# Kernel optimization log

Measured on AMD Instinct MI355X. Metric: run time of the kernel, lower is better.

## Reference

```python
import jax, jax.numpy as jnp
import numpy as np

S, N, D, H = 1024, 8, 1024, 16
DK = D // H
SCALE = np.sqrt(DK).astype(np.float32)


def setup_inputs() -> dict:
    key = jax.random.key(0)
    ks = jax.random.split(key, 16)
    f32 = jnp.float32
    Qpoi = jax.random.normal(ks[0], (S, N, D), f32)
    Qsvi = jax.random.normal(ks[1], (S, N, D), f32)
    K = jax.random.normal(ks[2], (S, N, D), f32)
    V = jax.random.normal(ks[3], (S, N, D), f32)
    # padding mask: True = masked key; random valid lengths in [S//2, S]
    lengths = jax.random.randint(ks[4], (N,), S // 2, S + 1)
    key_padding_mask = jnp.arange(S)[None, :] >= lengths[:, None]  # [N, S] bool
    w = 0.02
    wq_poi_w = jax.random.normal(ks[5], (D, D), f32) * w
    wq_poi_b = jnp.zeros((D,), f32)
    wq_svi_w = jax.random.normal(ks[6], (D, D), f32) * w
    wq_svi_b = jnp.zeros((D,), f32)
    wk_w = jax.random.normal(ks[7], (D, D), f32) * w
    wk_b = jnp.zeros((D,), f32)
    wv_w = jax.random.normal(ks[8], (D, D), f32) * w
    wv_b = jnp.zeros((D,), f32)
    fc_w = jax.random.normal(ks[9], (D, D), f32) * w
    fc_b = jnp.zeros((D,), f32)
    return dict(Qpoi=Qpoi, Qsvi=Qsvi, K=K, V=V, key_padding_mask=key_padding_mask,
                wq_poi_w=wq_poi_w, wq_poi_b=wq_poi_b, wq_svi_w=wq_svi_w, wq_svi_b=wq_svi_b,
                wk_w=wk_w, wk_b=wk_b, wv_w=wv_w, wv_b=wv_b, fc_w=fc_w, fc_b=fc_b)


def _proj_heads(x, W, b):
    # x: [S, N, D] -> linear -> [N, H, S, DK]
    y = x @ W.T + b                      # [S, N, D]
    y = jnp.transpose(y, (1, 0, 2))      # [N, S, D]
    y = y.reshape(N, S, H, DK)
    return jnp.transpose(y, (0, 2, 1, 3))  # [N, H, S, DK]


def _attend(Qh, Kh, Vh, mask):
    # Qh,Kh,Vh: [N, H, S, DK]; mask: [N, S] bool (True = masked)
    scores = jnp.einsum('nhqd,nhkd->nhqk', Qh, Kh) / SCALE
    scores = jnp.where(mask[:, None, None, :], -jnp.inf, scores)
    attn = jax.nn.softmax(scores, axis=-1)  # dropout is identity in eval
    out = jnp.einsum('nhqk,nhkd->nhqd', attn, Vh)
    out = jnp.transpose(out, (0, 2, 1, 3)).reshape(N, S, D)  # [N, S, D]
    return out


def reference(Qpoi, Qsvi, K, V, key_padding_mask,
              wq_poi_w, wq_poi_b, wq_svi_w, wq_svi_b,
              wk_w, wk_b, wv_w, wv_b, fc_w, fc_b):
    Qp = _proj_heads(Qpoi, wq_poi_w, wq_poi_b)
    Qs = _proj_heads(Qsvi, wq_svi_w, wq_svi_b)
    Kh = _proj_heads(K, wk_w, wk_b)
    Vh = _proj_heads(V, wv_w, wv_b)
    poi = _attend(Qp, Kh, Vh, key_padding_mask)
    svi = _attend(Qs, Kh, Vh, key_padding_mask)
    poi_out = jnp.transpose(poi @ fc_w.T + fc_b, (1, 0, 2))  # [S, N, D]
    svi_out = jnp.transpose(svi @ fc_w.T + fc_b, (1, 0, 2))
    return (poi_out, svi_out)
```

## Files before the change

kernel.cpp:

```cpp
#include <hip/hip_runtime.h>

typedef unsigned short u16;
typedef unsigned int u32;
typedef short bf16x8 __attribute__((ext_vector_type(8)));
typedef float f32x4 __attribute__((ext_vector_type(4)));

__device__ __forceinline__ u16 f2bf(float f) {
  union { float f; u32 i; } v; v.f = f;
  u32 x = v.i;
  return (u16)((x + 0x7fffu + ((x >> 16) & 1u)) >> 16);
}

union Pack16 { u16 h[16]; float4 f4[2]; };

__device__ __forceinline__ void gld16(const u16* g, u16* l) {
  __builtin_amdgcn_global_load_lds((const __attribute__((address_space(1))) u32*)g,
                                   (__attribute__((address_space(3))) u32*)l, 16, 0, 0);
}

__global__ __launch_bounds__(256) void conv_a_kernel(const float* __restrict__ src,
                                                     u16* __restrict__ dst) {
  const size_t i = (size_t)blockIdx.x * 256 + threadIdx.x;
  const float4* s = (const float4*)src + i * 2;
  float4 a = s[0], b = s[1];
  union { u16 h[8]; float4 f; } o;
  o.h[0] = f2bf(a.x); o.h[1] = f2bf(a.y); o.h[2] = f2bf(a.z); o.h[3] = f2bf(a.w);
  o.h[4] = f2bf(b.x); o.h[5] = f2bf(b.y); o.h[6] = f2bf(b.z); o.h[7] = f2bf(b.w);
  *(float4*)(dst + i * 8) = o.f;
}

struct W5 { const float* p[5]; };
__global__ __launch_bounds__(256) void conv_w_kernel(W5 w, u16* __restrict__ dst) {
  const int m = blockIdx.x >> 9;
  const size_t i = (size_t)(blockIdx.x & 511) * 256 + threadIdx.x;
  const float4* s = (const float4*)w.p[m] + i * 2;
  float4 a = s[0], b = s[1];
  union { u16 h[8]; float4 f; } o;
  o.h[0] = f2bf(a.x); o.h[1] = f2bf(a.y); o.h[2] = f2bf(a.z); o.h[3] = f2bf(a.w);
  o.h[4] = f2bf(b.x); o.h[5] = f2bf(b.y); o.h[6] = f2bf(b.z); o.h[7] = f2bf(b.w);
  *(float4*)(dst + ((size_t)m << 20) + i * 8) = o.f;
}

template<int ASRC>
__device__ __forceinline__ const u16* aAddr(const u16* A, int row, int k) {
  if constexpr (ASRC == 0) {
    return A + (size_t)row * 1024 + k;
  } else {
    const int n = row >> 10, s = row & 1023, h = k >> 6;
    return A + ((size_t)((n * 16 + h) * 1024 + s)) * 64 + (k & 63);
  }
}

template<int MODE, int ASRC, int WBF>
__global__ __launch_bounds__(256, 2) void gemm_bt(const void* __restrict__ A,
                                                  const void* __restrict__ W,
                                                  const float* __restrict__ bias,
                                                  void* __restrict__ outv) {
  __shared__ __align__(16) u16 At[128 * 32];
  __shared__ __align__(16) u16 Bt[128 * 32];

  const int tid = threadIdx.x;
  const int lane = tid & 63, wave = tid >> 6;
  const int quad = lane >> 4, l16 = lane & 15;
  const int bm = blockIdx.y * 128, bn = blockIdx.x * 128;
  const int wm = (wave >> 1) * 64, wn = (wave & 1) * 64;

  const int r0 = wave * 32;
  const int lrow = lane >> 2;
  const int lk = (lane & 3) * 8;

  const int srow = tid >> 1, scol = (tid & 1) * 16;

  const u16* Ab = (const u16*)A;
  const u16* Wb = (const u16*)W;

  f32x4 acc[4][4];
#pragma unroll
  for (int i = 0; i < 4; i++)
#pragma unroll
    for (int j = 0; j < 4; j++) acc[i][j] = (f32x4){0.f, 0.f, 0.f, 0.f};

  for (int k0 = 0; k0 < 1024; k0 += 32) {
    float4 wf[4];
    if constexpr (!WBF) {
      const float* wp = (const float*)W + (size_t)(bn + srow) * 1024 + k0 + scol;
#pragma unroll
      for (int q = 0; q < 4; q++) wf[q] = ((const float4*)wp)[q];
    }
    __syncthreads();
    gld16(aAddr<ASRC>(Ab, bm + r0 + lrow, k0 + lk), At + r0 * 32);
    gld16(aAddr<ASRC>(Ab, bm + r0 + 16 + lrow, k0 + lk), At + (r0 + 16) * 32);
    if constexpr (WBF) {
      gld16(Wb + (size_t)(bn + r0 + lrow) * 1024 + k0 + lk, Bt + r0 * 32);
      gld16(Wb + (size_t)(bn + r0 + 16 + lrow) * 1024 + k0 + lk, Bt + (r0 + 16) * 32);
    } else {
      Pack16 pb;
#pragma unroll
      for (int q = 0; q < 4; q++) {
        pb.h[q * 4 + 0] = f2bf(wf[q].x);
        pb.h[q * 4 + 1] = f2bf(wf[q].y);
        pb.h[q * 4 + 2] = f2bf(wf[q].z);
        pb.h[q * 4 + 3] = f2bf(wf[q].w);
      }
      *(float4*)(Bt + srow * 32 + scol) = pb.f4[0];
      *(float4*)(Bt + srow * 32 + scol + 8) = pb.f4[1];
    }
    __syncthreads();

    bf16x8 af[4], bfr[4];
#pragma unroll
    for (int mt = 0; mt < 4; mt++)
      af[mt] = *(const bf16x8*)(At + (wm + mt * 16 + l16) * 32 + quad * 8);
#pragma unroll
    for (int nt = 0; nt < 4; nt++)
      bfr[nt] = *(const bf16x8*)(Bt + (wn + nt * 16 + l16) * 32 + quad * 8);
#pragma unroll
    for (int mt = 0; mt < 4; mt++)
#pragma unroll
      for (int nt = 0; nt < 4; nt++)
        acc[mt][nt] = __builtin_amdgcn_mfma_f32_16x16x32_bf16(af[mt], bfr[nt], acc[mt][nt], 0, 0, 0);
  }

#pragma unroll
  for (int mt = 0; mt < 4; mt++) {
#pragma unroll
    for (int nt = 0; nt < 4; nt++) {
      const int col = bn + wn + nt * 16 + l16;
      const float bv = bias[col];
#pragma unroll
      for (int i = 0; i < 4; i++) {
        const int row = bm + wm + mt * 16 + quad * 4 + i;
        const float v = acc[mt][nt][i] + bv;
        if constexpr (MODE == 0) {
          const int s = row >> 3, n = row & 7;
          const int h = col >> 6, dk = col & 63;
          ((u16*)outv)[(size_t)(((n * 16 + h) * 1024 + s) * 64 + dk)] = f2bf(v);
        } else if constexpr (MODE == 1) {
          const int n = row >> 10, s = row & 1023;
          ((float*)outv)[(size_t)((s * 8 + n) * 1024 + col)] = v;
        } else {
          const int s = row >> 3, n = row & 7;
          const int h = col >> 6, dk = col & 63;
          ((u16*)outv)[(size_t)(((n * 16 + h) * 64 + dk) * 1024 + s)] = f2bf(v);
        }
      }
    }
  }
}

__global__ __launch_bounds__(256, 2) void attn2_kernel(const u16* __restrict__ Qs_g,
                                                       const u16* __restrict__ Qp_g,
                                                       const u16* __restrict__ K,
                                                       const u16* __restrict__ Vt_g,
                                                       const int* __restrict__ mask,
                                                       u16* __restrict__ OUTs,
                                                       u16* __restrict__ OUTp) {
  __shared__ __align__(16) u16 Ks[64 * 72];
  __shared__ __align__(16) u16 Vt[64 * 64];
  __shared__ __align__(16) u16 PsS[4 * 16 * 72];
  __shared__ __align__(16) u16 PsP[4 * 16 * 72];
  __shared__ float mbias[64];

  const int tid = threadIdx.x;
  const int lane = tid & 63, wave = tid >> 6;
  const int quad = lane >> 4, l16 = lane & 15;
  const int qt = blockIdx.x, nh = blockIdx.y;
  const int n = nh >> 4;
  const size_t base = (size_t)nh << 16;

  const int q0 = qt * 64 + wave * 16;
  bf16x8 qS0, qS1, qP0, qP1;
  {
    const u16* qp = Qs_g + base + (size_t)(q0 + l16) * 64 + quad * 8;
    qS0 = *(const bf16x8*)qp;
    qS1 = *(const bf16x8*)(qp + 32);
    const u16* qq = Qp_g + base + (size_t)(q0 + l16) * 64 + quad * 8;
    qP0 = *(const bf16x8*)qq;
    qP1 = *(const bf16x8*)(qq + 32);
  }

  float mS[4], mP[4];
  f32x4 oS[4], oP[4], lS, lP;
#pragma unroll
  for (int i = 0; i < 4; i++) { mS[i] = -1e30f; mP[i] = -1e30f; }
#pragma unroll
  for (int d = 0; d < 4; d++) { oS[d] = (f32x4){0.f, 0.f, 0.f, 0.f}; oP[d] = (f32x4){0.f, 0.f, 0.f, 0.f}; }
  lS = (f32x4){0.f, 0.f, 0.f, 0.f};
  lP = (f32x4){0.f, 0.f, 0.f, 0.f};

  bf16x8 vbOnes;
  {
    const short ob = (l16 == 0) ? (short)0x3F80 : (short)0;
#pragma unroll
    for (int j = 0; j < 8; j++) vbOnes[j] = ob;
  }

  const int sr = tid >> 2;
  const int sc = (tid & 3) * 16;
  const u16* kbase = K + base + (size_t)sr * 64 + sc;
  const u16* vbase = Vt_g + base + (size_t)sr * 1024 + sc;
  u16* vdst0 = Vt + sr * 64 + ((((sc >> 3) + 0) ^ (sr & 7)) << 3);
  u16* vdst1 = Vt + sr * 64 + ((((sc >> 3) + 1) ^ (sr & 7)) << 3);
  u16* pwS = PsS + wave * (16 * 72);
  u16* pwP = PsP + wave * (16 * 72);

  for (int kt = 0; kt < 16; kt++) {
    float4 kv0 = *(const float4*)(kbase + kt * 64 * 64);
    float4 kv1 = *(const float4*)(kbase + kt * 64 * 64 + 8);
    float4 vv0 = *(const float4*)(vbase + kt * 64);
    float4 vv1 = *(const float4*)(vbase + kt * 64 + 8);
    int mk = (tid < 64) ? mask[n * 1024 + kt * 64 + tid] : 0;
    __syncthreads();
    *(float4*)(Ks + sr * 72 + sc) = kv0;
    *(float4*)(Ks + sr * 72 + sc + 8) = kv1;
    *(float4*)vdst0 = vv0;
    *(float4*)vdst1 = vv1;
    if (tid < 64) mbias[tid] = mk ? -1e30f : 0.0f;
    __syncthreads();

    f32x4 sS[4], sP[4];
#pragma unroll
    for (int nt = 0; nt < 4; nt++) {
      bf16x8 b0 = *(const bf16x8*)(Ks + (nt * 16 + l16) * 72 + quad * 8);
      bf16x8 b1 = *(const bf16x8*)(Ks + (nt * 16 + l16) * 72 + 32 + quad * 8);
      f32x4 a = (f32x4){0.f, 0.f, 0.f, 0.f};
      a = __builtin_amdgcn_mfma_f32_16x16x32_bf16(qS0, b0, a, 0, 0, 0);
      a = __builtin_amdgcn_mfma_f32_16x16x32_bf16(qS1, b1, a, 0, 0, 0);
      sS[nt] = a;
      f32x4 c = (f32x4){0.f, 0.f, 0.f, 0.f};
      c = __builtin_amdgcn_mfma_f32_16x16x32_bf16(qP0, b0, c, 0, 0, 0);
      c = __builtin_amdgcn_mfma_f32_16x16x32_bf16(qP1, b1, c, 0, 0, 0);
      sP[nt] = c;
    }
    float mb[4];
#pragma unroll
    for (int nt = 0; nt < 4; nt++) mb[nt] = mbias[nt * 16 + l16];
#pragma unroll
    for (int nt = 0; nt < 4; nt++)
#pragma unroll
      for (int i = 0; i < 4; i++) {
        sS[nt][i] = sS[nt][i] * 0.125f + mb[nt];
        sP[nt][i] = sP[nt][i] * 0.125f + mb[nt];
      }

#pragma unroll
    for (int i = 0; i < 4; i++) {
      float m = fmaxf(fmaxf(sS[0][i], sS[1][i]), fmaxf(sS[2][i], sS[3][i]));
#pragma unroll
      for (int off = 1; off < 16; off <<= 1) m = fmaxf(m, __shfl_xor(m, off, 64));
      float mn = fmaxf(mS[i], m);
      float alpha = __expf(mS[i] - mn);
      mS[i] = mn;
#pragma unroll
      for (int d = 0; d < 4; d++) oS[d][i] *= alpha;
      lS[i] *= alpha;
    }
#pragma unroll
    for (int i = 0; i < 4; i++) {
      float m = fmaxf(fmaxf(sP[0][i], sP[1][i]), fmaxf(sP[2][i], sP[3][i]));
#pragma unroll
      for (int off = 1; off < 16; off <<= 1) m = fmaxf(m, __shfl_xor(m, off, 64));
      float mn = fmaxf(mP[i], m);
      float alpha = __expf(mP[i] - mn);
      mP[i] = mn;
#pragma unroll
      for (int d = 0; d < 4; d++) oP[d][i] *= alpha;
      lP[i] *= alpha;
    }
#pragma unroll
    for (int nt = 0; nt < 4; nt++)
#pragma unroll
      for (int i = 0; i < 4; i++) {
        pwS[(quad * 4 + i) * 72 + nt * 16 + l16] = f2bf(__expf(sS[nt][i] - mS[i]));
        pwP[(quad * 4 + i) * 72 + nt * 16 + l16] = f2bf(__expf(sP[nt][i] - mP[i]));
      }
    __syncthreads();

#pragma unroll
    for (int ks = 0; ks < 2; ks++) {
      bf16x8 paS = *(const bf16x8*)(pwS + l16 * 72 + ks * 32 + quad * 8);
      bf16x8 paP = *(const bf16x8*)(pwP + l16 * 72 + ks * 32 + quad * 8);
      lS = __builtin_amdgcn_mfma_f32_16x16x32_bf16(paS, vbOnes, lS, 0, 0, 0);
      lP = __builtin_amdgcn_mfma_f32_16x16x32_bf16(paP, vbOnes, lP, 0, 0, 0);
#pragma unroll
      for (int d = 0; d < 4; d++) {
        bf16x8 vb = *(const bf16x8*)(Vt + (d * 16 + l16) * 64 +
                                     (((ks * 4 + quad) ^ (l16 & 7)) << 3));
        oS[d] = __builtin_amdgcn_mfma_f32_16x16x32_bf16(paS, vb, oS[d], 0, 0, 0);
        oP[d] = __builtin_amdgcn_mfma_f32_16x16x32_bf16(paP, vb, oP[d], 0, 0, 0);
      }
    }
  }

#pragma unroll
  for (int i = 0; i < 4; i++) {
    const float lsv = __shfl(lS[i], lane & 48, 64);
    const float lpv = __shfl(lP[i], lane & 48, 64);
    const float invS = 1.0f / lsv;
    const float invP = 1.0f / lpv;
    const int q = q0 + quad * 4 + i;
    const size_t ob = base + (size_t)q * 64;
#pragma unroll
    for (int d = 0; d < 4; d++) {
      OUTs[ob + d * 16 + l16] = f2bf(oS[d][i] * invS);
      OUTp[ob + d * 16 + l16] = f2bf(oP[d][i] * invP);
    }
  }
}

extern "C" void kernel_launch(void* const* d_in, const int* in_sizes, int n_in,
                              void* d_out, int out_size, void* d_ws, size_t ws_size,
                              hipStream_t stream) {
  const float* Qpoi = (const float*)d_in[0];
  const float* Qsvi = (const float*)d_in[1];
  const float* Kin  = (const float*)d_in[2];
  const float* Vin  = (const float*)d_in[3];
  const int* mask   = (const int*)d_in[4];
  const float* wq_poi_w = (const float*)d_in[5];
  const float* wq_poi_b = (const float*)d_in[6];
  const float* wq_svi_w = (const float*)d_in[7];
  const float* wq_svi_b = (const float*)d_in[8];
  const float* wk_w = (const float*)d_in[9];
  const float* wk_b = (const float*)d_in[10];
  const float* wv_w = (const float*)d_in[11];
  const float* wv_b = (const float*)d_in[12];
  const float* fc_w = (const float*)d_in[13];
  const float* fc_b = (const float*)d_in[14];

  const size_t SZ = (size_t)8 * 16 * 1024 * 64;
  const size_t WBE = (size_t)5 << 20;
  u16* W0 = (u16*)d_ws;
  u16* W1 = W0 + SZ;
  u16* W2 = W1 + SZ;
  const bool haveWb = ws_size >= (2 * SZ + WBE) * sizeof(u16);
  const bool haveW2 = ws_size >= (3 * SZ + WBE) * sizeof(u16);
  u16* WbWs = haveW2 ? (W2 + SZ) : (W1 + SZ);

  float* Of = (float*)d_out;
  u16* R0 = (u16*)d_out;
  u16* R1 = R0 + SZ;
  u16* R2 = R0 + 2 * SZ;
  u16* R3 = R0 + 3 * SZ;

  u16* Wp = haveWb ? WbWs : R1;

  dim3 bb(256, 1, 1);
  dim3 gg(8, 64);
  dim3 ga(16, 128);
  dim3 gc(4096);

  {
    W5 w5{{wk_w, wv_w, wq_svi_w, wq_poi_w, fc_w}};
    const int nm = haveWb ? 5 : 4;
    hipLaunchKernelGGL(conv_w_kernel, dim3(nm * 512), bb, 0, stream, w5, Wp);
  }
  const u16* Wk  = Wp + ((size_t)0 << 20);
  const u16* Wv  = Wp + ((size_t)1 << 20);
  const u16* Wqs = Wp + ((size_t)2 << 20);
  const u16* Wqp = Wp + ((size_t)3 << 20);

  hipLaunchKernelGGL(conv_a_kernel, gc, bb, 0, stream, Kin, R0);
  hipLaunchKernelGGL((gemm_bt<0, 0, 1>), gg, bb, 0, stream, (const void*)R0, (const void*)Wk, wk_b, (void*)W0);
  hipLaunchKernelGGL(conv_a_kernel, gc, bb, 0, stream, Vin, R0);
  hipLaunchKernelGGL((gemm_bt<2, 0, 1>), gg, bb, 0, stream, (const void*)R0, (const void*)Wv, wv_b, (void*)W1);
  hipLaunchKernelGGL(conv_a_kernel, gc, bb, 0, stream, Qsvi, R0);
  hipLaunchKernelGGL((gemm_bt<0, 0, 1>), gg, bb, 0, stream, (const void*)R0, (const void*)Wqs, wq_svi_b, (void*)R2);
  hipLaunchKernelGGL(conv_a_kernel, gc, bb, 0, stream, Qpoi, R0);
  hipLaunchKernelGGL((gemm_bt<0, 0, 1>), gg, bb, 0, stream, (const void*)R0, (const void*)Wqp, wq_poi_b, (void*)R3);

  u16* ctx_svi = haveW2 ? W2 : R2;
  hipLaunchKernelGGL(attn2_kernel, ga, bb, 0, stream,
                     (const u16*)R2, (const u16*)R3, (const u16*)W0, (const u16*)W1,
                     mask, ctx_svi, R3);

  if (haveWb) {
    const u16* Wfc = Wp + ((size_t)4 << 20);
    hipLaunchKernelGGL((gemm_bt<1, 1, 1>), gg, bb, 0, stream, (const void*)R3, (const void*)Wfc, fc_b, (void*)Of);
    if (haveW2) {
      hipLaunchKernelGGL((gemm_bt<1, 1, 1>), gg, bb, 0, stream, (const void*)W2, (const void*)Wfc, fc_b, (void*)(Of + SZ));
    } else {
      hipMemcpyAsync(W0, R2, SZ * sizeof(u16), hipMemcpyDeviceToDevice, stream);
      hipLaunchKernelGGL((gemm_bt<1, 1, 1>), gg, bb, 0, stream, (const void*)W0, (const void*)Wfc, fc_b, (void*)(Of + SZ));
    }
  } else {
    hipLaunchKernelGGL((gemm_bt<1, 1, 0>), gg, bb, 0, stream, (const void*)R3, (const void*)fc_w, fc_b, (void*)Of);
    hipMemcpyAsync(W0, R2, SZ * sizeof(u16), hipMemcpyDeviceToDevice, stream);
    hipLaunchKernelGGL((gemm_bt<1, 1, 0>), gg, bb, 0, stream, (const void*)W0, (const void*)fc_w, fc_b, (void*)(Of + SZ));
  }
}
```

Measured before the change: 547.2 us.

## Batch paired conversions and GEMMs into single launches via grid z-dimension

Merges the K/V and Qsvi/Qpoi fp32-to-bf16 conversions and their projection GEMMs into paired launches that use blockIdx.z to pick operands, and does the same for the two output fc GEMMs. The aim is to cut launch count and fill the GPU with twice as many blocks per launch. In exchange, the fc stage now copies both attention contexts into workspace with two device-to-device memcpys, adding extra memory traffic. The GEMM epilogue mode becomes a runtime branch rather than a compile-time constant.

```diff
diff --git a/kernel.cpp b/kernel.cpp
--- a/kernel.cpp
+++ b/kernel.cpp
@@ -18,15 +18,16 @@
                                    (__attribute__((address_space(3))) u32*)l, 16, 0, 0);
 }
 
-__global__ __launch_bounds__(256) void conv_a_kernel(const float* __restrict__ src,
-                                                     u16* __restrict__ dst) {
+struct C2 { const float* s[2]; u16* d[2]; };
+__global__ __launch_bounds__(256) void conv2_kernel(C2 c) {
+  const int z = blockIdx.z;
   const size_t i = (size_t)blockIdx.x * 256 + threadIdx.x;
-  const float4* s = (const float4*)src + i * 2;
+  const float4* s = (const float4*)c.s[z] + i * 2;
   float4 a = s[0], b = s[1];
   union { u16 h[8]; float4 f; } o;
   o.h[0] = f2bf(a.x); o.h[1] = f2bf(a.y); o.h[2] = f2bf(a.z); o.h[3] = f2bf(a.w);
   o.h[4] = f2bf(b.x); o.h[5] = f2bf(b.y); o.h[6] = f2bf(b.z); o.h[7] = f2bf(b.w);
-  *(float4*)(dst + i * 8) = o.f;
+  *(float4*)(c.d[z] + i * 8) = o.f;
 }
 
 struct W5 { const float* p[5]; };
@@ -51,13 +52,19 @@
   }
 }
 
-template<int MODE, int ASRC, int WBF>
-__global__ __launch_bounds__(256, 2) void gemm_bt(const void* __restrict__ A,
-                                                  const void* __restrict__ W,
-                                                  const float* __restrict__ bias,
-                                                  void* __restrict__ outv) {
+struct GB { const void* A[2]; const void* W[2]; const float* bias[2]; void* out[2]; };
+
+template<int MODEA, int MODEB, int ASRC, int WBF>
+__global__ __launch_bounds__(256, 2) void gemm_bt(GB gb) {
   __shared__ __align__(16) u16 At[128 * 32];
   __shared__ __align__(16) u16 Bt[128 * 32];
+
+  const int z = blockIdx.z;
+  const u16* Ab = (const u16*)gb.A[z];
+  const u16* Wb = (const u16*)gb.W[z];
+  const float* bias = gb.bias[z];
+  void* outv = gb.out[z];
+  const int mode = z ? MODEB : MODEA;
 
   const int tid = threadIdx.x;
   const int lane = tid & 63, wave = tid >> 6;
@@ -71,9 +78,6 @@
 
   const int srow = tid >> 1, scol = (tid & 1) * 16;
 
-  const u16* Ab = (const u16*)A;
-  const u16* Wb = (const u16*)W;
-
   f32x4 acc[4][4];
 #pragma unroll
   for (int i = 0; i < 4; i++)
@@ -83,7 +87,7 @@
   for (int k0 = 0; k0 < 1024; k0 += 32) {
     float4 wf[4];
     if constexpr (!WBF) {
-      const float* wp = (const float*)W + (size_t)(bn + srow) * 1024 + k0 + scol;
+      const float* wp = (const float*)Wb + (size_t)(bn + srow) * 1024 + k0 + scol;
 #pragma unroll
       for (int q = 0; q < 4; q++) wf[q] = ((const float4*)wp)[q];
     }
@@ -131,11 +135,11 @@
       for (int i = 0; i < 4; i++) {
         const int row = bm + wm + mt * 16 + quad * 4 + i;
         const float v = acc[mt][nt][i] + bv;
-        if constexpr (MODE == 0) {
+        if (mode == 0) {
           const int s = row >> 3, n = row & 7;
           const int h = col >> 6, dk = col & 63;
           ((u16*)outv)[(size_t)(((n * 16 + h) * 1024 + s) * 64 + dk)] = f2bf(v);
-        } else if constexpr (MODE == 1) {
+        } else if (mode == 1) {
           const int n = row >> 10, s = row & 1023;
           ((float*)outv)[(size_t)((s * 8 + n) * 1024 + col)] = v;
         } else {
@@ -331,10 +335,8 @@
   const size_t WBE = (size_t)5 << 20;
   u16* W0 = (u16*)d_ws;
   u16* W1 = W0 + SZ;
-  u16* W2 = W1 + SZ;
+  u16* Wp = W1 + SZ;
   const bool haveWb = ws_size >= (2 * SZ + WBE) * sizeof(u16);
-  const bool haveW2 = ws_size >= (3 * SZ + WBE) * sizeof(u16);
-  u16* WbWs = haveW2 ? (W2 + SZ) : (W1 + SZ);
 
   float* Of = (float*)d_out;
   u16* R0 = (u16*)d_out;
@@ -342,49 +344,52 @@
   u16* R2 = R0 + 2 * SZ;
   u16* R3 = R0 + 3 * SZ;
 
-  u16* Wp = haveWb ? WbWs : R1;
-
   dim3 bb(256, 1, 1);
-  dim3 gg(8, 64);
+  dim3 gg(8, 64, 2);
   dim3 ga(16, 128);
-  dim3 gc(4096);
-
-  {
+  dim3 gc(4096, 1, 2);
+
+  if (haveWb) {
     W5 w5{{wk_w, wv_w, wq_svi_w, wq_poi_w, fc_w}};
-    const int nm = haveWb ? 5 : 4;
-    hipLaunchKernelGGL(conv_w_kernel, dim3(nm * 512), bb, 0, stream, w5, Wp);
+    hipLaunchKernelGGL(conv_w_kernel, dim3(2560), bb, 0, stream, w5, Wp);
   }
   const u16* Wk  = Wp + ((size_t)0 << 20);
   const u16* Wv  = Wp + ((size_t)1 << 20);
   const u16* Wqs = Wp + ((size_t)2 << 20);
   const u16* Wqp = Wp + ((size_t)3 << 20);
-
-  hipLaunchKernelGGL(conv_a_kernel, gc, bb, 0, stream, Kin, R0);
-  hipLaunchKernelGGL((gemm_bt<0, 0, 1>), gg, bb, 0, stream, (const void*)R0, (const void*)Wk, wk_b, (void*)W0);
-  hipLaunchKernelGGL(conv_a_kernel, gc, bb, 0, stream, Vin, R0);
-  hipLaunchKernelGGL((gemm_bt<2, 0, 1>), gg, bb, 0, stream, (const void*)R0, (const void*)Wv, wv_b, (void*)W1);
-  hipLaunchKernelGGL(conv_a_kernel, gc, bb, 0, stream, Qsvi, R0);
-  hipLaunchKernelGGL((gemm_bt<0, 0, 1>), gg, bb, 0, stream, (const void*)R0, (const void*)Wqs, wq_svi_b, (void*)R2);
-  hipLaunchKernelGGL(conv_a_kernel, gc, bb, 0, stream, Qpoi, R0);
-  hipLaunchKernelGGL((gemm_bt<0, 0, 1>), gg, bb, 0, stream, (const void*)R0, (const void*)Wqp, wq_poi_b, (void*)R3);
-
-  u16* ctx_svi = haveW2 ? W2 : R2;
+  const u16* Wfc = Wp + ((size_t)4 << 20);
+
+  {
+    C2 c{{Kin, Vin}, {R0, R1}};
+    hipLaunchKernelGGL(conv2_kernel, gc, bb, 0, stream, c);
+    GB g{{R0, R1},
+         {haveWb ? (const void*)Wk : (const void*)wk_w, haveWb ? (const void*)Wv : (const void*)wv_w},
+         {wk_b, wv_b}, {(void*)W0, (void*)W1}};
+    if (haveWb) hipLaunchKernelGGL((gemm_bt<0, 2, 0, 1>), gg, bb, 0, stream, g);
+    else        hipLaunchKernelGGL((gemm_bt<0, 2, 0, 0>), gg, bb, 0, stream, g);
+  }
+
+  {
+    C2 c{{Qsvi, Qpoi}, {R0, R1}};
+    hipLaunchKernelGGL(conv2_kernel, gc, bb, 0, stream, c);
+    GB g{{R0, R1},
+         {haveWb ? (const void*)Wqs : (const void*)wq_svi_w, haveWb ? (const void*)Wqp : (const void*)wq_poi_w},
+         {wq_svi_b, wq_poi_b}, {(void*)R2, (void*)R3}};
+    if (haveWb) hipLaunchKernelGGL((gemm_bt<0, 0, 0, 1>), gg, bb, 0, stream, g);
+    else        hipLaunchKernelGGL((gemm_bt<0, 0, 0, 0>), gg, bb, 0, stream, g);
+  }
+
   hipLaunchKernelGGL(attn2_kernel, ga, bb, 0, stream,
                      (const u16*)R2, (const u16*)R3, (const u16*)W0, (const u16*)W1,
-                     mask, ctx_svi, R3);
-
-  if (haveWb) {
-    const u16* Wfc = Wp + ((size_t)4 << 20);
-    hipLaunchKernelGGL((gemm_bt<1, 1, 1>), gg, bb, 0, stream, (const void*)R3, (const void*)Wfc, fc_b, (void*)Of);
-    if (haveW2) {
-      hipLaunchKernelGGL((gemm_bt<1, 1, 1>), gg, bb, 0, stream, (const void*)W2, (const void*)Wfc, fc_b, (void*)(Of + SZ));
-    } else {
-      hipMemcpyAsync(W0, R2, SZ * sizeof(u16), hipMemcpyDeviceToDevice, stream);
-      hipLaunchKernelGGL((gemm_bt<1, 1, 1>), gg, bb, 0, stream, (const void*)W0, (const void*)Wfc, fc_b, (void*)(Of + SZ));
-    }
-  } else {
-    hipLaunchKernelGGL((gemm_bt<1, 1, 0>), gg, bb, 0, stream, (const void*)R3, (const void*)fc_w, fc_b, (void*)Of);
-    hipMemcpyAsync(W0, R2, SZ * sizeof(u16), hipMemcpyDeviceToDevice, stream);
-    hipLaunchKernelGGL((gemm_bt<1, 1, 0>), gg, bb, 0, stream, (const void*)W0, (const void*)fc_w, fc_b, (void*)(Of + SZ));
-  }
-}
+                     mask, R2, R3);
+
+  hipMemcpyAsync(W0, R3, SZ * sizeof(u16), hipMemcpyDeviceToDevice, stream);
+  hipMemcpyAsync(W1, R2, SZ * sizeof(u16), hipMemcpyDeviceToDevice, stream);
+  {
+    GB g{{W0, W1},
+         {haveWb ? (const void*)Wfc : (const void*)fc_w, haveWb ? (const void*)Wfc : (const void*)fc_w},
+         {fc_b, fc_b}, {(void*)Of, (void*)(Of + SZ)}};
+    if (haveWb) hipLaunchKernelGGL((gemm_bt<1, 1, 1, 1>), gg, bb, 0, stream, g);
+    else        hipLaunchKernelGGL((gemm_bt<1, 1, 1, 0>), gg, bb, 0, stream, g);
+  }
+}
```

New measurement: 534.6 us. -2.3%, faster.
